# Kernel optimization log

Measured on AMD Instinct MI355X. Metric: run time of the kernel, lower is better.

The kernel has to match this reference:

```python
import jax, jax.numpy as jnp
import numpy as np
from jax import lax

H = 128


def _ema_scan(x):
    # x: [B, T, N, F] -> EMA along T: s_t = 0.9*s_{t-1} + 0.1*x_t
    xt = jnp.moveaxis(x, 1, 0)  # [T, B, N, F]

    def step(s, xi):
        s = s * 0.9 + xi * 0.1
        return s, s

    _, ys = lax.scan(step, jnp.zeros_like(xt[0]), xt)
    return jnp.moveaxis(ys, 0, 1)  # [B, T, N, F]


def setup_inputs() -> dict:
    key = jax.random.key(0)
    k1, k2, k3, k4, k5 = jax.random.split(key, 5)
    B, T, N = 4, 96, 512
    x = jax.random.normal(k1, (B, T, N, H), dtype=jnp.float32)
    s = 1.0 / np.sqrt(H)
    W_exp = jax.random.uniform(k2, (2 * H, H), jnp.float32, -s, s)
    b_exp = jax.random.uniform(k3, (2 * H,), jnp.float32, -s, s)
    W_con = jax.random.uniform(k4, (H, H), jnp.float32, -s, s)
    b_con = jax.random.uniform(k5, (H,), jnp.float32, -s, s)
    return {"spatial_temporal_representation": x, "W_exp": W_exp, "b_exp": b_exp,
            "W_con": W_con, "b_con": b_con}


def reference(spatial_temporal_representation, W_exp, b_exp, W_con, b_con):
    x = spatial_temporal_representation  # [B,T,N,H]
    expanded = jnp.einsum('btnh,oh->btno', x, W_exp) + b_exp  # [B,T,N,2H]
    state_primary, state_gating = jnp.split(expanded, 2, axis=-1)
    gated_activation = jax.nn.sigmoid(_ema_scan(state_gating))
    out = jnp.einsum('btnh,oh->btno', state_primary * gated_activation, W_con) + b_con
    return out
```

## Files before the change

### kernel.cpp

```cpp
#include <hip/hip_runtime.h>

#define B_DIM 4
#define T_DIM 96
#define N_DIM 512
#define H_DIM 128
#define NH    (N_DIM * H_DIM)

#define WS_WEXP  0
#define WS_WCON  32768
#define WS_L     49152
#define WS_TOTAL 58368

typedef __attribute__((ext_vector_type(8))) short short8;
typedef __attribute__((ext_vector_type(4))) float f32x4;

__device__ __forceinline__ unsigned short f2b_rh(float f) {
    union { float f; unsigned u; } c; c.f = f;
    return (unsigned short)((c.u + 0x8000u) >> 16);
}
__device__ __forceinline__ unsigned pack_bf16_2(float a, float b) {
    union { float f; unsigned u; } ca, cb; ca.f = a; cb.f = b;
    return __builtin_amdgcn_perm(cb.u + 0x8000u, ca.u + 0x8000u, 0x07060302u);
}
__device__ __forceinline__ float u2f(unsigned u) {
    union { unsigned u; float f; } c; c.u = u;
    return c.f;
}

extern "C" __global__ void prep_kernel(const float* __restrict__ Wexp,
                                       const float* __restrict__ Wcon,
                                       unsigned short* __restrict__ ws) {
    int i = blockIdx.x * 256 + threadIdx.x;
    if (i < 32768) {
        ws[WS_WEXP + i] = f2b_rh(Wexp[i]);
    } else if (i < 49152) {
        int j = i - 32768;
        ws[WS_WCON + j] = f2b_rh(Wcon[j]);
    } else if (i < WS_TOTAL) {
        int j = i - 49152;
        int t = j / 96, k = j - t * 96;
        float v = 0.0f;
        if (k <= t) v = 0.1f * __expf((float)(t - k) * -0.1053605157f);
        ws[WS_L + j] = f2b_rh(v);
    }
}

extern "C" __global__ __launch_bounds__(256, 3)
void mamba_fused(const float* __restrict__ x,
                 const unsigned short* __restrict__ ws,
                 const float* __restrict__ b_exp,
                 const float* __restrict__ b_con,
                 float* __restrict__ out)
{
    __shared__ __align__(16) unsigned short gpg[128 * 104];

    const int tid  = threadIdx.x;
    const int wave = tid >> 6;
    const int lane = tid & 63;
    const int q    = lane >> 4;
    const int l16  = lane & 15;

    const int blk = blockIdx.x;
    const int n   = blk & (N_DIM - 1);
    const int b   = blk >> 9;

    const float* xg = x + ((size_t)b * T_DIM * N_DIM + (size_t)n) * H_DIM;

    short8 wp[2][4], wg[2][4];
    #pragma unroll
    for (int ot = 0; ot < 2; ++ot) {
        const unsigned short* wrp = ws + WS_WEXP + (size_t)((wave * 2 + ot) * 16 + l16) * H_DIM + q * 8;
        #pragma unroll
        for (int k0 = 0; k0 < 4; ++k0) {
            wp[ot][k0] = *(const short8*)(wrp + k0 * 32);
            wg[ot][k0] = *(const short8*)(wrp + 128 * H_DIM + k0 * 32);
        }
    }

    unsigned pacc[2][6][2];

    #pragma unroll
    for (int mt = 0; mt < 6; ++mt) {
        const float* xrow = xg + (size_t)(mt * 16 + l16) * NH + q * 8;
        short8 bfr[4];
        #pragma unroll
        for (int k0 = 0; k0 < 4; ++k0) {
            float4 v0 = *(const float4*)(xrow + k0 * 32);
            float4 v1 = *(const float4*)(xrow + k0 * 32 + 4);
            union { unsigned u[4]; short8 s; } p;
            p.u[0] = pack_bf16_2(v0.x, v0.y);
            p.u[1] = pack_bf16_2(v0.z, v0.w);
            p.u[2] = pack_bf16_2(v1.x, v1.y);
            p.u[3] = pack_bf16_2(v1.z, v1.w);
            bfr[k0] = p.s;
        }
        f32x4 ap0 = {0.f,0.f,0.f,0.f}, ap1 = {0.f,0.f,0.f,0.f};
        f32x4 ag0 = {0.f,0.f,0.f,0.f}, ag1 = {0.f,0.f,0.f,0.f};
        #pragma unroll
        for (int k0 = 0; k0 < 4; ++k0) {
            ap0 = __builtin_amdgcn_mfma_f32_16x16x32_bf16(wp[0][k0], bfr[k0], ap0, 0, 0, 0);
            ap1 = __builtin_amdgcn_mfma_f32_16x16x32_bf16(wp[1][k0], bfr[k0], ap1, 0, 0, 0);
            ag0 = __builtin_amdgcn_mfma_f32_16x16x32_bf16(wg[0][k0], bfr[k0], ag0, 0, 0, 0);
            ag1 = __builtin_amdgcn_mfma_f32_16x16x32_bf16(wg[1][k0], bfr[k0], ag1, 0, 0, 0);
        }
        pacc[0][mt][0] = pack_bf16_2(ap0[0], ap0[1]);
        pacc[0][mt][1] = pack_bf16_2(ap0[2], ap0[3]);
        pacc[1][mt][0] = pack_bf16_2(ap1[0], ap1[1]);
        pacc[1][mt][1] = pack_bf16_2(ap1[2], ap1[3]);
        unsigned short* gr0 = &gpg[((wave * 2 + 0) * 16 + q * 4) * 104 + mt * 16 + l16];
        gr0[0]       = f2b_rh(ag0[0]);
        gr0[104]     = f2b_rh(ag0[1]);
        gr0[2 * 104] = f2b_rh(ag0[2]);
        gr0[3 * 104] = f2b_rh(ag0[3]);
        unsigned short* gr1 = &gpg[((wave * 2 + 1) * 16 + q * 4) * 104 + mt * 16 + l16];
        gr1[0]       = f2b_rh(ag1[0]);
        gr1[104]     = f2b_rh(ag1[1]);
        gr1[2 * 104] = f2b_rh(ag1[2]);
        gr1[3 * 104] = f2b_rh(ag1[3]);
    }

    asm volatile("s_waitcnt lgkmcnt(0)" ::: "memory");
    __builtin_amdgcn_sched_barrier(0);

    f32x4 eacc[2][6];
    #pragma unroll
    for (int ht = 0; ht < 2; ++ht)
        #pragma unroll
        for (int tt = 0; tt < 6; ++tt)
            eacc[ht][tt] = (f32x4){0.f, 0.f, 0.f, 0.f};
    {
        const unsigned short* wsL = ws + WS_L;
        #pragma unroll
        for (int kf = 0; kf < 3; ++kf) {
            short8 af0 = *(const short8*)&gpg[((wave * 2 + 0) * 16 + l16) * 104 + kf * 32 + q * 8];
            short8 af1 = *(const short8*)&gpg[((wave * 2 + 1) * 16 + l16) * 104 + kf * 32 + q * 8];
            #pragma unroll
            for (int tt = 0; tt < 6; ++tt) {
                if (tt < 2 * kf) continue;
                short8 bf = *(const short8*)(wsL + (size_t)(tt * 16 + l16) * 96 + kf * 32 + q * 8);
                eacc[0][tt] = __builtin_amdgcn_mfma_f32_16x16x32_bf16(af0, bf, eacc[0][tt], 0, 0, 0);
                eacc[1][tt] = __builtin_amdgcn_mfma_f32_16x16x32_bf16(af1, bf, eacc[1][tt], 0, 0, 0);
            }
        }
    }

    float4 bp[2], bgv[2];
    #pragma unroll
    for (int ot = 0; ot < 2; ++ot) {
        const int o = (wave * 2 + ot) * 16;
        bp[ot]  = *(const float4*)(b_exp + o + q * 4);
        bgv[ot] = *(const float4*)(b_exp + 128 + o + q * 4);
    }
    float cfac[6];
    #pragma unroll
    for (int tt = 0; tt < 6; ++tt)
        cfac[tt] = 1.0f - __expf((float)(tt * 16 + l16 + 1) * -0.1053605157f);

    __syncthreads();

    #pragma unroll
    for (int ot = 0; ot < 2; ++ot) {
        const int hb = (wave * 2 + ot) * 16 + q * 4;
        #pragma unroll
        for (int tt = 0; tt < 6; ++tt) {
            const int t = tt * 16 + l16;
            f32x4 s = eacc[ot][tt];
            float sg0 = __fdividef(1.f, 1.f + __expf(-(s[0] + bgv[ot].x * cfac[tt])));
            float sg1 = __fdividef(1.f, 1.f + __expf(-(s[1] + bgv[ot].y * cfac[tt])));
            float sg2 = __fdividef(1.f, 1.f + __expf(-(s[2] + bgv[ot].z * cfac[tt])));
            float sg3 = __fdividef(1.f, 1.f + __expf(-(s[3] + bgv[ot].w * cfac[tt])));
            unsigned u0 = pacc[ot][tt][0], u1 = pacc[ot][tt][1];
            float p0 = (u2f(u0 << 16)         + bp[ot].x) * sg0;
            float p1 = (u2f(u0 & 0xffff0000u) + bp[ot].y) * sg1;
            float p2 = (u2f(u1 << 16)         + bp[ot].z) * sg2;
            float p3 = (u2f(u1 & 0xffff0000u) + bp[ot].w) * sg3;
            union { unsigned u[2]; ushort4 s; } pk;
            pk.u[0] = pack_bf16_2(p0, p1);
            pk.u[1] = pack_bf16_2(p2, p3);
            *(ushort4*)&gpg[t * 136 + hb] = pk.s;
        }
    }

    short8 wc[2][4];
    float4 bias2[2];
    #pragma unroll
    for (int ot = 0; ot < 2; ++ot) {
        const int o = (wave * 2 + ot) * 16;
        const unsigned short* wrc = ws + WS_WCON + (size_t)(o + l16) * H_DIM + q * 8;
        #pragma unroll
        for (int k0 = 0; k0 < 4; ++k0)
            wc[ot][k0] = *(const short8*)(wrc + k0 * 32);
        bias2[ot] = *(const float4*)(b_con + o + q * 4);
    }
    __syncthreads();

    float* og = out + ((size_t)b * T_DIM * N_DIM + (size_t)n) * H_DIM;
    #pragma unroll
    for (int mt = 0; mt < 6; ++mt) {
        short8 bfr[4];
        const unsigned short* prow = &gpg[(mt * 16 + l16) * 136];
        #pragma unroll
        for (int k0 = 0; k0 < 4; ++k0)
            bfr[k0] = *(const short8*)(prow + k0 * 32 + q * 8);
        const int t = mt * 16 + l16;
        #pragma unroll
        for (int ot = 0; ot < 2; ++ot) {
            f32x4 acc = {0.f, 0.f, 0.f, 0.f};
            #pragma unroll
            for (int k0 = 0; k0 < 4; ++k0)
                acc = __builtin_amdgcn_mfma_f32_16x16x32_bf16(wc[ot][k0], bfr[k0], acc, 0, 0, 0);
            const int o = (wave * 2 + ot) * 16 + q * 4;
            float4 v;
            v.x = acc[0] + bias2[ot].x;
            v.y = acc[1] + bias2[ot].y;
            v.z = acc[2] + bias2[ot].z;
            v.w = acc[3] + bias2[ot].w;
            *(float4*)(og + (size_t)t * NH + o) = v;
        }
    }
}

extern "C" void kernel_launch(void* const* d_in, const int* in_sizes, int n_in,
                              void* d_out, int out_size, void* d_ws, size_t ws_size,
                              hipStream_t stream) {
    const float* x     = (const float*)d_in[0];
    const float* W_exp = (const float*)d_in[1];
    const float* b_exp = (const float*)d_in[2];
    const float* W_con = (const float*)d_in[3];
    const float* b_con = (const float*)d_in[4];
    float* out = (float*)d_out;
    unsigned short* ws = (unsigned short*)d_ws;

    hipLaunchKernelGGL(prep_kernel, dim3(WS_TOTAL / 256), dim3(256), 0, stream,
                       W_exp, W_con, ws);
    hipLaunchKernelGGL(mamba_fused, dim3(B_DIM * N_DIM), dim3(256), 0, stream,
                       x, ws, b_exp, b_con, out);
}
```

Measured before the change: 243.9 us.

## Stage x tiles cooperatively through double-buffered LDS with register prefetch

Previously each of the four waves loaded and converted the full 16x128 fp32 x tile itself, so every tile was fetched four times. Now all 256 threads load each tile once, convert it to bf16, and store it into a double-buffered LDS staging area, with the tile two steps ahead already held in registers. Each wave then reads its MFMA operands from LDS. Row strides of the LDS buffers (GS, XS) also change to shift bank patterns. This cuts redundant global and L1 traffic and conversion work, at the cost of one workgroup barrier per time tile and extra LDS use.

```diff
diff --git a/kernel.cpp b/kernel.cpp
--- a/kernel.cpp
+++ b/kernel.cpp
@@ -11,6 +11,9 @@
 #define WS_L     49152
 #define WS_TOTAL 58368
 
+#define XS 132
+#define GS 100
+
 typedef __attribute__((ext_vector_type(8))) short short8;
 typedef __attribute__((ext_vector_type(4))) float f32x4;
 
@@ -26,6 +29,13 @@
     union { unsigned u; float f; } c; c.u = u;
     return c.f;
 }
+
+#define BAR_LGKM()  do {                                        \
+    asm volatile("s_waitcnt lgkmcnt(0)" ::: "memory");          \
+    __builtin_amdgcn_sched_barrier(0);                          \
+    __builtin_amdgcn_s_barrier();                               \
+    __builtin_amdgcn_sched_barrier(0);                          \
+} while (0)
 
 extern "C" __global__ void prep_kernel(const float* __restrict__ Wexp,
                                        const float* __restrict__ Wcon,
@@ -52,7 +62,8 @@
                  const float* __restrict__ b_con,
                  float* __restrict__ out)
 {
-    __shared__ __align__(16) unsigned short gpg[128 * 104];
+    __shared__ __align__(16) unsigned short xw[2][16 * XS];
+    __shared__ __align__(16) unsigned short gpg[128 * GS];
 
     const int tid  = threadIdx.x;
     const int wave = tid >> 6;
@@ -66,6 +77,19 @@
 
     const float* xg = x + ((size_t)b * T_DIM * N_DIM + (size_t)n) * H_DIM;
 
+    const int srow = tid >> 4;
+    const int scol = (tid & 15) * 8;
+
+    float4 vx[2][2];
+    {
+        const float* xr0 = xg + (size_t)srow * NH + scol;
+        vx[0][0] = *(const float4*)xr0;
+        vx[0][1] = *(const float4*)(xr0 + 4);
+        const float* xr1 = xg + (size_t)(16 + srow) * NH + scol;
+        vx[1][0] = *(const float4*)xr1;
+        vx[1][1] = *(const float4*)(xr1 + 4);
+    }
+
     short8 wp[2][4], wg[2][4];
     #pragma unroll
     for (int ot = 0; ot < 2; ++ot) {
@@ -81,19 +105,27 @@
 
     #pragma unroll
     for (int mt = 0; mt < 6; ++mt) {
-        const float* xrow = xg + (size_t)(mt * 16 + l16) * NH + q * 8;
+        const int sl = mt & 1;
+        {
+            union { unsigned u[2]; ushort4 s; } p0, p1;
+            p0.u[0] = pack_bf16_2(vx[sl][0].x, vx[sl][0].y);
+            p0.u[1] = pack_bf16_2(vx[sl][0].z, vx[sl][0].w);
+            p1.u[0] = pack_bf16_2(vx[sl][1].x, vx[sl][1].y);
+            p1.u[1] = pack_bf16_2(vx[sl][1].z, vx[sl][1].w);
+            *(ushort4*)&xw[sl][srow * XS + scol]     = p0.s;
+            *(ushort4*)&xw[sl][srow * XS + scol + 4] = p1.s;
+        }
+        if (mt + 2 < 6) {
+            const float* xr = xg + (size_t)((mt + 2) * 16 + srow) * NH + scol;
+            vx[sl][0] = *(const float4*)xr;
+            vx[sl][1] = *(const float4*)(xr + 4);
+        }
+        BAR_LGKM();
+
         short8 bfr[4];
         #pragma unroll
-        for (int k0 = 0; k0 < 4; ++k0) {
-            float4 v0 = *(const float4*)(xrow + k0 * 32);
-            float4 v1 = *(const float4*)(xrow + k0 * 32 + 4);
-            union { unsigned u[4]; short8 s; } p;
-            p.u[0] = pack_bf16_2(v0.x, v0.y);
-            p.u[1] = pack_bf16_2(v0.z, v0.w);
-            p.u[2] = pack_bf16_2(v1.x, v1.y);
-            p.u[3] = pack_bf16_2(v1.z, v1.w);
-            bfr[k0] = p.s;
-        }
+        for (int k0 = 0; k0 < 4; ++k0)
+            bfr[k0] = *(const short8*)&xw[sl][l16 * XS + k0 * 32 + q * 8];
         f32x4 ap0 = {0.f,0.f,0.f,0.f}, ap1 = {0.f,0.f,0.f,0.f};
         f32x4 ag0 = {0.f,0.f,0.f,0.f}, ag1 = {0.f,0.f,0.f,0.f};
         #pragma unroll
@@ -107,16 +139,16 @@
         pacc[0][mt][1] = pack_bf16_2(ap0[2], ap0[3]);
         pacc[1][mt][0] = pack_bf16_2(ap1[0], ap1[1]);
         pacc[1][mt][1] = pack_bf16_2(ap1[2], ap1[3]);
-        unsigned short* gr0 = &gpg[((wave * 2 + 0) * 16 + q * 4) * 104 + mt * 16 + l16];
-        gr0[0]       = f2b_rh(ag0[0]);
-        gr0[104]     = f2b_rh(ag0[1]);
-        gr0[2 * 104] = f2b_rh(ag0[2]);
-        gr0[3 * 104] = f2b_rh(ag0[3]);
-        unsigned short* gr1 = &gpg[((wave * 2 + 1) * 16 + q * 4) * 104 + mt * 16 + l16];
-        gr1[0]       = f2b_rh(ag1[0]);
-        gr1[104]     = f2b_rh(ag1[1]);
-        gr1[2 * 104] = f2b_rh(ag1[2]);
-        gr1[3 * 104] = f2b_rh(ag1[3]);
+        unsigned short* gr0 = &gpg[((wave * 2 + 0) * 16 + q * 4) * GS + mt * 16 + l16];
+        gr0[0]      = f2b_rh(ag0[0]);
+        gr0[GS]     = f2b_rh(ag0[1]);
+        gr0[2 * GS] = f2b_rh(ag0[2]);
+        gr0[3 * GS] = f2b_rh(ag0[3]);
+        unsigned short* gr1 = &gpg[((wave * 2 + 1) * 16 + q * 4) * GS + mt * 16 + l16];
+        gr1[0]      = f2b_rh(ag1[0]);
+        gr1[GS]     = f2b_rh(ag1[1]);
+        gr1[2 * GS] = f2b_rh(ag1[2]);
+        gr1[3 * GS] = f2b_rh(ag1[3]);
     }
 
     asm volatile("s_waitcnt lgkmcnt(0)" ::: "memory");
@@ -132,8 +164,8 @@
         const unsigned short* wsL = ws + WS_L;
         #pragma unroll
         for (int kf = 0; kf < 3; ++kf) {
-            short8 af0 = *(const short8*)&gpg[((wave * 2 + 0) * 16 + l16) * 104 + kf * 32 + q * 8];
-            short8 af1 = *(const short8*)&gpg[((wave * 2 + 1) * 16 + l16) * 104 + kf * 32 + q * 8];
+            short8 af0 = *(const short8*)&gpg[((wave * 2 + 0) * 16 + l16) * GS + kf * 32 + q * 8];
+            short8 af1 = *(const short8*)&gpg[((wave * 2 + 1) * 16 + l16) * GS + kf * 32 + q * 8];
             #pragma unroll
             for (int tt = 0; tt < 6; ++tt) {
                 if (tt < 2 * kf) continue;
@@ -156,7 +188,7 @@
     for (int tt = 0; tt < 6; ++tt)
         cfac[tt] = 1.0f - __expf((float)(tt * 16 + l16 + 1) * -0.1053605157f);
 
-    __syncthreads();
+    BAR_LGKM();
 
     #pragma unroll
     for (int ot = 0; ot < 2; ++ot) {
@@ -177,7 +209,7 @@
             union { unsigned u[2]; ushort4 s; } pk;
             pk.u[0] = pack_bf16_2(p0, p1);
             pk.u[1] = pack_bf16_2(p2, p3);
-            *(ushort4*)&gpg[t * 136 + hb] = pk.s;
+            *(ushort4*)&gpg[t * XS + hb] = pk.s;
         }
     }
 
@@ -192,13 +224,13 @@
             wc[ot][k0] = *(const short8*)(wrc + k0 * 32);
         bias2[ot] = *(const float4*)(b_con + o + q * 4);
     }
-    __syncthreads();
+    BAR_LGKM();
 
     float* og = out + ((size_t)b * T_DIM * N_DIM + (size_t)n) * H_DIM;
     #pragma unroll
     for (int mt = 0; mt < 6; ++mt) {
         short8 bfr[4];
-        const unsigned short* prow = &gpg[(mt * 16 + l16) * 136];
+        const unsigned short* prow = &gpg[(mt * 16 + l16) * XS];
         #pragma unroll
         for (int k0 = 0; k0 < 4; ++k0)
             bfr[k0] = *(const short8*)(prow + k0 * 32 + q * 8);
```

New measurement: 211.7 us. -13.2%, faster.
